# Kernel optimization log

Hardware: AMD Instinct MI355X
Metric: run time of the kernel (lower is better)

The kernel has to match this reference:

```python
import jax, jax.numpy as jnp
import numpy as np

B, T, E = 64, 64, 512
D_MODEL = 2 * E          # 1024, mamba d_model (concat of spatial+temporal)
D_INNER = 2 * D_MODEL    # 2048
D_STATE = 16
DT_RANK = D_MODEL // 16  # 64
K_CONV = 4


def setup_inputs() -> dict:
    key = jax.random.key(0)
    ks = jax.random.split(key, 12)
    def n(k, shape, scale=0.02):
        return jax.random.normal(k, shape, jnp.float32) * scale
    return {
        "spatial_features": jax.random.normal(ks[0], (B, T, E), jnp.float32),
        "temporal_features": jax.random.normal(ks[1], (B, T, E), jnp.float32),
        "W_in": n(ks[2], (D_MODEL, 2 * D_INNER)),
        "conv_w": n(ks[3], (D_INNER, K_CONV)),
        "conv_b": jnp.zeros((D_INNER,), jnp.float32),
        "W_x": n(ks[4], (D_INNER, DT_RANK + 2 * D_STATE)),
        "W_dt": n(ks[5], (DT_RANK, D_INNER)),
        "b_dt": jnp.zeros((D_INNER,), jnp.float32),
        "A_log": n(ks[6], (D_INNER, D_STATE)),   # A = -exp(A_log) ~ -1
        "D_skip": jnp.ones((D_INNER,), jnp.float32),
        "W_out": n(ks[7], (D_INNER, D_MODEL)),
        "W1": n(ks[8], (D_MODEL, 512)),
        "b1": jnp.zeros((512,), jnp.float32),
        "W2": n(ks[9], (512, 256)),
        "b2": jnp.zeros((256,), jnp.float32),
        "W3": n(ks[10], (256, 6)),
        "b3": jnp.zeros((6,), jnp.float32),
    }


def _mamba(x, W_in, conv_w, conv_b, W_x, W_dt, b_dt, A_log, D_skip, W_out):
    # x: (B, T, d_model) -> (B, T, d_model). Standard Mamba selective-scan block.
    Bsz = x.shape[0]
    xz = jnp.einsum('btd,de->bte', x, W_in)            # (B,T,2*d_inner)
    xi, z = jnp.split(xz, 2, axis=-1)
    # causal depthwise conv1d over T
    xt = jnp.pad(jnp.swapaxes(xi, 1, 2), ((0, 0), (0, 0), (K_CONV - 1, 0)))
    conv = jax.lax.conv_general_dilated(
        xt, conv_w[:, None, :], (1,), 'VALID', feature_group_count=D_INNER)
    xc = jax.nn.silu(jnp.swapaxes(conv, 1, 2) + conv_b)  # (B,T,d_inner)
    proj = jnp.einsum('btd,de->bte', xc, W_x)            # (B,T,dt_rank+2n)
    dt_raw, Bs, Cs = jnp.split(proj, [DT_RANK, DT_RANK + D_STATE], axis=-1)
    dt = jax.nn.softplus(jnp.einsum('btr,rd->btd', dt_raw, W_dt) + b_dt)
    A = -jnp.exp(A_log)                                  # (d_inner, n)

    def step(h, inputs):
        dt_t, B_t, C_t, x_t = inputs                     # (B,d),(B,n),(B,n),(B,d)
        dA = jnp.exp(dt_t[..., None] * A)                # (B,d,n)
        h = dA * h + (dt_t * x_t)[..., None] * B_t[:, None, :]
        y = jnp.einsum('bdn,bn->bd', h, C_t)
        return h, y

    xs = (jnp.swapaxes(dt, 0, 1), jnp.swapaxes(Bs, 0, 1),
          jnp.swapaxes(Cs, 0, 1), jnp.swapaxes(xc, 0, 1))
    h0 = jnp.zeros((Bsz, D_INNER, D_STATE), xc.dtype)
    _, ys = jax.lax.scan(step, h0, xs)
    y = jnp.swapaxes(ys, 0, 1) + xc * D_skip
    y = y * jax.nn.silu(z)
    return jnp.einsum('btd,de->bte', y, W_out)


def reference(spatial_features, temporal_features, W_in, conv_w, conv_b, W_x,
              W_dt, b_dt, A_log, D_skip, W_out, W1, b1, W2, b2, W3, b3):
    # concat -> final Mamba -> per-frame MLP head (vectorized over B,T)
    x = jnp.concatenate([spatial_features, temporal_features], axis=-1)  # (B,T,2E)
    f = _mamba(x, W_in, conv_w, conv_b, W_x, W_dt, b_dt, A_log, D_skip, W_out)
    h1 = jax.nn.relu(f @ W1 + b1)
    h2 = jax.nn.relu(h1 @ W2 + b2)
    return h2 @ W3 + b3  # (B,T,6)
```

## Files before the change

kernel.cpp:

```cpp
#include <hip/hip_runtime.h>
#include <hip/hip_bf16.h>
#include <math.h>

#define B_   64
#define T_   64
#define E_   512
#define DM   1024
#define DI   2048
#define DS   16
#define DTR  64
#define M_   4096

typedef __hip_bfloat16 bf16;
typedef __attribute__((ext_vector_type(8))) short bf16x8;
typedef __attribute__((ext_vector_type(4))) float f32x4;

template<int ACT, int OUTBF, int SPLITK, int BM, int BN, int ATOMIC = 0>
__global__ __launch_bounds__(256) void gemm_mfma(
    const bf16* __restrict__ A, int lda,
    const bf16* __restrict__ Bt, int ldb,
    void* __restrict__ Cv, int ldc,
    const float* __restrict__ bias,
    int Ndim, int Kdim)
{
    __shared__ __align__(16) bf16 As[BM * 32];
    __shared__ __align__(16) bf16 Bs[BN * 32];
    const int tid  = threadIdx.x;
    const int wave = tid >> 6;
    const int lane = tid & 63;
    const int bm = blockIdx.y * BM;
    const int bn = blockIdx.x * BN;
    const int lrow = lane >> 2;
    const int lkc  = (lane & 3) * 8;
    constexpr int RPW = (BM + BN) / 4;
    constexpr int NI  = RPW / 16;
    constexpr int WMT = BM / 32;
    constexpr int WNT = BN / 32;
    const int wm = (wave >> 1) * (BM / 2);
    const int wn = (wave & 1) * (BN / 2);
    const int fm = lane & 15;
    const int fq = lane >> 4;

    int kstart = 0, kend = Kdim;
    if (SPLITK > 1) {
        int chunk = Kdim / SPLITK;
        kstart = blockIdx.z * chunk;
        kend = kstart + chunk;
    }

    f32x4 acc[WMT][WNT];
    #pragma unroll
    for (int i = 0; i < WMT; ++i)
        #pragma unroll
        for (int j = 0; j < WNT; ++j)
            acc[i][j] = (f32x4){0.f, 0.f, 0.f, 0.f};

    for (int k0 = kstart; k0 < kend; k0 += 32) {
        #pragma unroll
        for (int i = 0; i < NI; ++i) {
            int rowbase = wave * RPW + i * 16;
            int row = rowbase + lrow;
            if (rowbase < BM) {
                const bf16* ga = A + (size_t)(bm + row) * lda + k0 + lkc;
                __builtin_amdgcn_global_load_lds(
                    (const __attribute__((address_space(1))) void*)ga,
                    (__attribute__((address_space(3))) void*)&As[rowbase * 32],
                    16, 0, 0);
            } else {
                int brow = bn + row - BM;
                if (brow >= Ndim) brow = Ndim - 1;
                const bf16* gb = Bt + (size_t)brow * ldb + k0 + lkc;
                __builtin_amdgcn_global_load_lds(
                    (const __attribute__((address_space(1))) void*)gb,
                    (__attribute__((address_space(3))) void*)&Bs[(rowbase - BM) * 32],
                    16, 0, 0);
            }
        }
        __syncthreads();
        bf16x8 a[WMT], b[WNT];
        #pragma unroll
        for (int i = 0; i < WMT; ++i)
            a[i] = *(const bf16x8*)&As[(wm + i * 16 + fm) * 32 + fq * 8];
        #pragma unroll
        for (int j = 0; j < WNT; ++j)
            b[j] = *(const bf16x8*)&Bs[(wn + j * 16 + fm) * 32 + fq * 8];
        #pragma unroll
        for (int i = 0; i < WMT; ++i)
            #pragma unroll
            for (int j = 0; j < WNT; ++j)
                acc[i][j] = __builtin_amdgcn_mfma_f32_16x16x32_bf16(
                    a[i], b[j], acc[i][j], 0, 0, 0);
        __syncthreads();
    }

    size_t zoff = (SPLITK > 1 && !ATOMIC) ? (size_t)blockIdx.z * M_ * ldc : 0;
    #pragma unroll
    for (int i = 0; i < WMT; ++i) {
        int rowb = bm + wm + i * 16 + fq * 4;
        #pragma unroll
        for (int j = 0; j < WNT; ++j) {
            int col = bn + wn + j * 16 + fm;
            if (col < Ndim) {
                float bv = bias ? bias[col] : 0.f;
                #pragma unroll
                for (int r = 0; r < 4; ++r) {
                    float v = acc[i][j][r] + bv;
                    if (ACT == 1) v = fmaxf(v, 0.f);
                    if (ACT == 2) v = (v > 20.f) ? v : __logf(1.f + __expf(v));
                    size_t off = (size_t)(rowb + r) * ldc + col;
                    if (ATOMIC)          atomicAdd(&((float*)Cv)[off], v);
                    else if (SPLITK > 1) ((float*)Cv)[zoff + off] = v;
                    else if (OUTBF)      ((bf16*)Cv)[off] = __float2bfloat16(v);
                    else                 ((float*)Cv)[off] = v;
                }
            }
        }
    }
}

__global__ __launch_bounds__(256) void gemm_g1_conv(
    const bf16* __restrict__ A,
    const bf16* __restrict__ Bt,
    bf16* __restrict__ xcb,
    bf16* __restrict__ zb,
    const float* __restrict__ conv_w,
    const float* __restrict__ conv_b,
    const bf16* __restrict__ W1T,
    const bf16* __restrict__ Wob,
    bf16* __restrict__ WcT)
{
    constexpr int XS = 136;
    __shared__ __align__(16) bf16 smem[128 * XS];
    const int tid  = threadIdx.x;
    const int wave = tid >> 6;
    const int lane = tid & 63;
    const int lrow = lane >> 2;
    const int lkc  = (lane & 3) * 8;
    const int wm = (wave >> 1) * 64;
    const int fm = lane & 15;
    const int fq = lane >> 4;

    if (blockIdx.x >= 32) {
        const int fbm = (blockIdx.x - 32) * 128;
        const int fbn = blockIdx.y * 64;
        const int fwn = (wave & 1) * 32;
        f32x4 facc[4][2];
        #pragma unroll
        for (int i = 0; i < 4; ++i)
            #pragma unroll
            for (int j = 0; j < 2; ++j)
                facc[i][j] = (f32x4){0.f, 0.f, 0.f, 0.f};

        for (int k0 = 0; k0 < 1024; k0 += 32) {
            #pragma unroll
            for (int i = 0; i < 3; ++i) {
                int rowbase = wave * 48 + i * 16;
                int row = rowbase + lrow;
                if (rowbase < 128) {
                    const bf16* ga = W1T + (size_t)(fbm + row) * 1024 + k0 + lkc;
                    __builtin_amdgcn_global_load_lds(
                        (const __attribute__((address_space(1))) void*)ga,
                        (__attribute__((address_space(3))) void*)&smem[rowbase * 32],
                        16, 0, 0);
                } else {
                    const bf16* gb = Wob + (size_t)(fbn + row - 128) * 1024 + k0 + lkc;
                    __builtin_amdgcn_global_load_lds(
                        (const __attribute__((address_space(1))) void*)gb,
                        (__attribute__((address_space(3))) void*)&smem[4096 + (rowbase - 128) * 32],
                        16, 0, 0);
                }
            }
            __syncthreads();
            bf16x8 a[4], b[2];
            #pragma unroll
            for (int i = 0; i < 4; ++i)
                a[i] = *(const bf16x8*)&smem[(wm + i * 16 + fm) * 32 + fq * 8];
            #pragma unroll
            for (int j = 0; j < 2; ++j)
                b[j] = *(const bf16x8*)&smem[4096 + (fwn + j * 16 + fm) * 32 + fq * 8];
            #pragma unroll
            for (int i = 0; i < 4; ++i)
                #pragma unroll
                for (int j = 0; j < 2; ++j)
                    facc[i][j] = __builtin_amdgcn_mfma_f32_16x16x32_bf16(
                        a[i], b[j], facc[i][j], 0, 0, 0);
            __syncthreads();
        }
        #pragma unroll
        for (int i = 0; i < 4; ++i) {
            int rowb = fbm + wm + i * 16 + fq * 4;
            #pragma unroll
            for (int j = 0; j < 2; ++j) {
                int col = fbn + fwn + j * 16 + fm;
                #pragma unroll
                for (int r = 0; r < 4; ++r)
                    WcT[(size_t)(rowb + r) * 2048 + col] =
                        __float2bfloat16(facc[i][j][r]);
            }
        }
        return;
    }

    const int bm = blockIdx.y * 128;
    const int bn = blockIdx.x * 128;
    const int wn = (wave & 1) * 64;

    f32x4 acc[4][4];
    #pragma unroll
    for (int i = 0; i < 4; ++i)
        #pragma unroll
        for (int j = 0; j < 4; ++j)
            acc[i][j] = (f32x4){0.f, 0.f, 0.f, 0.f};

    for (int k0 = 0; k0 < 1024; k0 += 32) {
        #pragma unroll
        for (int i = 0; i < 4; ++i) {
            int rowbase = wave * 64 + i * 16;
            int row = rowbase + lrow;
            if (rowbase < 128) {
                const bf16* ga = A + (size_t)(bm + row) * 1024 + k0 + lkc;
                __builtin_amdgcn_global_load_lds(
                    (const __attribute__((address_space(1))) void*)ga,
                    (__attribute__((address_space(3))) void*)&smem[rowbase * 32],
                    16, 0, 0);
            } else {
                const bf16* gb = Bt + (size_t)(bn + row - 128) * 1024 + k0 + lkc;
                __builtin_amdgcn_global_load_lds(
                    (const __attribute__((address_space(1))) void*)gb,
                    (__attribute__((address_space(3))) void*)&smem[4096 + (rowbase - 128) * 32],
                    16, 0, 0);
            }
        }
        __syncthreads();
        bf16x8 a[4], b[4];
        #pragma unroll
        for (int i = 0; i < 4; ++i)
            a[i] = *(const bf16x8*)&smem[(wm + i * 16 + fm) * 32 + fq * 8];
        #pragma unroll
        for (int j = 0; j < 4; ++j)
            b[j] = *(const bf16x8*)&smem[4096 + (wn + j * 16 + fm) * 32 + fq * 8];
        #pragma unroll
        for (int i = 0; i < 4; ++i)
            #pragma unroll
            for (int j = 0; j < 4; ++j)
                acc[i][j] = __builtin_amdgcn_mfma_f32_16x16x32_bf16(
                    a[i], b[j], acc[i][j], 0, 0, 0);
        __syncthreads();
    }

    if (bn < 2048) {
        #pragma unroll
        for (int i = 0; i < 4; ++i) {
            int rowb = wm + i * 16 + fq * 4;
            #pragma unroll
            for (int j = 0; j < 4; ++j) {
                int col = wn + j * 16 + fm;
                #pragma unroll
                for (int r = 0; r < 4; ++r)
                    smem[(rowb + r) * XS + col] = __float2bfloat16(acc[i][j][r]);
            }
        }
        __syncthreads();
        {
            int col = tid & 127;
            int seq = tid >> 7;
            int gcol = bn + col;
            float4 cw = *(const float4*)&conv_w[gcol * 4];
            float cb = conv_b[gcol];
            float w0 = 0.f, w1 = 0.f, w2 = 0.f;
            int base = seq * 64;
            for (int t = 0; t < 64; ++t) {
                int idx = (base + t) * XS + col;
                float cur = __bfloat162float(smem[idx]);
                float cacc = cb;
                cacc = fmaf(w0, cw.x, cacc); cacc = fmaf(w1, cw.y, cacc);
                cacc = fmaf(w2, cw.z, cacc); cacc = fmaf(cur, cw.w, cacc);
                smem[idx] = __float2bfloat16(__fdividef(cacc, 1.f + __expf(-cacc)));
                w0 = w1; w1 = w2; w2 = cur;
            }
        }
        __syncthreads();
        #pragma unroll
        for (int it = 0; it < 8; ++it) {
            int g = it * 256 + tid;
            int row = g >> 4;
            int cg = (g & 15) * 8;
            bf16x8 v = *(const bf16x8*)&smem[row * XS + cg];
            *(bf16x8*)&xcb[(size_t)(bm + row) * 2048 + bn + cg] = v;
        }
    } else {
        #pragma unroll
        for (int i = 0; i < 4; ++i) {
            int rowb = bm + wm + i * 16 + fq * 4;
            #pragma unroll
            for (int j = 0; j < 4; ++j) {
                int col = bn - 2048 + wn + j * 16 + fm;
                #pragma unroll
                for (int r = 0; r < 4; ++r)
                    zb[(size_t)(rowb + r) * 2048 + col] =
                        __float2bfloat16(acc[i][j][r]);
            }
        }
    }
}

__global__ __launch_bounds__(256) void gemm_g3(
    const float* __restrict__ proj,
    const bf16* __restrict__ WdT,
    bf16* __restrict__ dtb,
    const float* __restrict__ b_dt)
{
    __shared__ __align__(16) bf16 As[128 * 32];
    __shared__ __align__(16) bf16 Bs[64 * 32];
    const int tid  = threadIdx.x;
    const int wave = tid >> 6;
    const int lane = tid & 63;
    const int bm = blockIdx.y * 128;
    const int bn = blockIdx.x * 64;
    const int lrow = lane >> 2;
    const int lkc  = (lane & 3) * 8;
    const int wm = (wave >> 1) * 64;
    const int wn = (wave & 1) * 32;
    const int fm = lane & 15;
    const int fq = lane >> 4;
    const int arow = tid >> 1;
    const int akh  = (tid & 1) * 16;

    f32x4 acc[4][2];
    #pragma unroll
    for (int i = 0; i < 4; ++i)
        #pragma unroll
        for (int j = 0; j < 2; ++j)
            acc[i][j] = (f32x4){0.f, 0.f, 0.f, 0.f};

    #pragma unroll
    for (int k0 = 0; k0 < 64; k0 += 32) {
        {
            const bf16* gb = WdT + (size_t)(bn + wave * 16 + lrow) * 64 + k0 + lkc;
            __builtin_amdgcn_global_load_lds(
                (const __attribute__((address_space(1))) void*)gb,
                (__attribute__((address_space(3))) void*)&Bs[wave * 16 * 32],
                16, 0, 0);
        }
        {
            const float* ga = proj + (size_t)(bm + arow) * 96 + k0 + akh;
            float4 v0 = *(const float4*)(ga + 0);
            float4 v1 = *(const float4*)(ga + 4);
            float4 v2 = *(const float4*)(ga + 8);
            float4 v3 = *(const float4*)(ga + 12);
            bf16 o[16] = {
                __float2bfloat16(v0.x), __float2bfloat16(v0.y),
                __float2bfloat16(v0.z), __float2bfloat16(v0.w),
                __float2bfloat16(v1.x), __float2bfloat16(v1.y),
                __float2bfloat16(v1.z), __float2bfloat16(v1.w),
                __float2bfloat16(v2.x), __float2bfloat16(v2.y),
                __float2bfloat16(v2.z), __float2bfloat16(v2.w),
                __float2bfloat16(v3.x), __float2bfloat16(v3.y),
                __float2bfloat16(v3.z), __float2bfloat16(v3.w)};
            *(bf16x8*)&As[arow * 32 + akh]     = *(const bf16x8*)&o[0];
            *(bf16x8*)&As[arow * 32 + akh + 8] = *(const bf16x8*)&o[8];
        }
        __syncthreads();
        bf16x8 a[4], b[2];
        #pragma unroll
        for (int i = 0; i < 4; ++i)
            a[i] = *(const bf16x8*)&As[(wm + i * 16 + fm) * 32 + fq * 8];
        #pragma unroll
        for (int j = 0; j < 2; ++j)
            b[j] = *(const bf16x8*)&Bs[(wn + j * 16 + fm) * 32 + fq * 8];
        #pragma unroll
        for (int i = 0; i < 4; ++i)
            #pragma unroll
            for (int j = 0; j < 2; ++j)
                acc[i][j] = __builtin_amdgcn_mfma_f32_16x16x32_bf16(
                    a[i], b[j], acc[i][j], 0, 0, 0);
        __syncthreads();
    }

    #pragma unroll
    for (int i = 0; i < 4; ++i) {
        int rowb = bm + wm + i * 16 + fq * 4;
        #pragma unroll
        for (int j = 0; j < 2; ++j) {
            int col = bn + wn + j * 16 + fm;
            float bv = b_dt[col];
            #pragma unroll
            for (int r = 0; r < 4; ++r) {
                float v = acc[i][j][r] + bv;
                v = (v > 20.f) ? v : __logf(1.f + __expf(v));
                dtb[(size_t)(rowb + r) * 2048 + col] = __float2bfloat16(v);
            }
        }
    }
}

template<int P, int RELU, int NCOL>
__global__ __launch_bounds__(256) void redp_kernel(
    const float* __restrict__ parts, int stride,
    const float* __restrict__ bias, bf16* __restrict__ out)
{
    int i4 = blockIdx.x * 256 + threadIdx.x;
    int i = i4 * 4;
    float4 s = *(const float4*)(parts + i);
    #pragma unroll
    for (int p = 1; p < P; ++p) {
        float4 v = *(const float4*)(parts + (size_t)p * stride + i);
        s.x += v.x; s.y += v.y; s.z += v.z; s.w += v.w;
    }
    if (NCOL > 0) {
        int c = i & (NCOL - 1);
        s.x += bias[c]; s.y += bias[c + 1]; s.z += bias[c + 2]; s.w += bias[c + 3];
    }
    if (RELU) {
        s.x = fmaxf(s.x, 0.f); s.y = fmaxf(s.y, 0.f);
        s.z = fmaxf(s.z, 0.f); s.w = fmaxf(s.w, 0.f);
    }
    bf16 o[4] = {__float2bfloat16(s.x), __float2bfloat16(s.y),
                 __float2bfloat16(s.z), __float2bfloat16(s.w)};
    *(short4*)&out[i] = *(short4*)o;
}

__global__ __launch_bounds__(256) void prep_kernel(
    const float* __restrict__ sp, const float* __restrict__ tp,
    bf16* __restrict__ xb, float* __restrict__ proj,
    const float* __restrict__ W_in,  bf16* __restrict__ WinT,
    const float* __restrict__ W_out, bf16* __restrict__ Wob,
    const float* __restrict__ W_x,   bf16* __restrict__ WxT,
    const float* __restrict__ W_dt,  bf16* __restrict__ WdT,
    const float* __restrict__ W1,    bf16* __restrict__ W1T,
    const float* __restrict__ W2,    bf16* __restrict__ W2T)
{
    __shared__ float tile[32][33];
    const int b = blockIdx.x;
    const int tid = threadIdx.x;
    if (b < 4096) {
        int idx = b * 256 + tid;
        int row = idx >> 8;
        int c4 = (idx & 255) * 4;
        const float* src = (c4 < 512) ? (sp + (size_t)row * 512 + c4)
                                      : (tp + (size_t)row * 512 + (c4 - 512));
        float4 v = *(const float4*)src;
        bf16* dst = xb + (size_t)row * 1024 + c4;
        dst[0] = __float2bfloat16(v.x); dst[1] = __float2bfloat16(v.y);
        dst[2] = __float2bfloat16(v.z); dst[3] = __float2bfloat16(v.w);
        if (idx < 98304)
            *(float4*)(proj + (size_t)idx * 4) = make_float4(0.f, 0.f, 0.f, 0.f);
        return;
    }
    if (b < 6144) {
        int idx = (b - 4096) * 1024 + tid * 4;
        float4 v = *(const float4*)(W_out + idx);
        bf16 o[4] = {__float2bfloat16(v.x), __float2bfloat16(v.y),
                     __float2bfloat16(v.z), __float2bfloat16(v.w)};
        *(short4*)&Wob[idx] = *(short4*)o;
        return;
    }
    const float* W; bf16* Wt; int K, N, tb;
    if      (b < 6336) { W = W_x;  Wt = WxT;  K = 2048; N = 96;   tb = b - 6144; }
    else if (b < 6464) { W = W_dt; Wt = WdT;  K = 64;   N = 2048; tb = b - 6336; }
    else if (b < 6976) { W = W1;   Wt = W1T;  K = 1024; N = 512;  tb = b - 6464; }
    else if (b < 7104) { W = W2;   Wt = W2T;  K = 512;  N = 256;  tb = b - 6976; }
    else               { W = W_in; Wt = WinT; K = 1024; N = 4096; tb = b - 7104; }
    int nb = N / 32;
    int bn = (tb % nb) * 32, bk = (tb / nb) * 32;
    int tx = tid & 31, ty = tid >> 5;
    #pragma unroll
    for (int i = 0; i < 32; i += 8)
        tile[ty + i][tx] = W[(size_t)(bk + ty + i) * N + bn + tx];
    __syncthreads();
    #pragma unroll
    for (int i = 0; i < 32; i += 8)
        Wt[(size_t)(bn + ty + i) * K + bk + tx] = __float2bfloat16(tile[tx][ty + i]);
}

__global__ __launch_bounds__(256) void scan_kernel(
    const float* __restrict__ proj,
    const bf16*  __restrict__ dtb,
    bf16* __restrict__ xcy,
    const bf16*  __restrict__ zb,
    const float* __restrict__ A_log,
    const float* __restrict__ D_skip)
{
    __shared__ float BC[64][32];
    const int tid = threadIdx.x;
    const int b = blockIdx.y;
    for (int i = tid; i < 64 * 32; i += 256) {
        int t = i >> 5, c = i & 31;
        BC[t][c] = proj[(size_t)(b * 64 + t) * 96 + 64 + c];
    }
    __syncthreads();

    const int d = blockIdx.x * 256 + tid;
    float av[16];
    const float4* alp = (const float4*)(A_log + d * 16);
    *(float4*)&av[0]  = alp[0];
    *(float4*)&av[4]  = alp[1];
    *(float4*)&av[8]  = alp[2];
    *(float4*)&av[12] = alp[3];
    float A[16];
    #pragma unroll
    for (int n = 0; n < 16; ++n) A[n] = -__expf(av[n]);
    const float Dv = D_skip[d];
    float h[16];
    #pragma unroll
    for (int n = 0; n < 16; ++n) h[n] = 0.f;

    #pragma unroll 2
    for (int t = 0; t < T_; ++t) {
        int row = b * T_ + t;
        size_t off = (size_t)row * DI + d;
        float xv = __bfloat162float(xcy[off]);
        float dt = __bfloat162float(dtb[off]);
        float dtx = dt * xv;
        float y = 0.f;
        #pragma unroll
        for (int n = 0; n < 16; ++n) {
            float dA = __expf(dt * A[n]);
            h[n] = fmaf(dA, h[n], dtx * BC[t][n]);
            y = fmaf(h[n], BC[t][16 + n], y);
        }
        float sk = fmaf(xv, Dv, y);
        float z = __bfloat162float(zb[off]);
        float g = __fdividef(z, 1.f + __expf(-z));
        xcy[off] = __float2bfloat16(sk * g);
    }
}

template<int P>
__global__ __launch_bounds__(256) void head_kernel(
    const float* __restrict__ p6, int stride,
    const float* __restrict__ b2,
    const float* __restrict__ W3, const float* __restrict__ b3,
    float* __restrict__ out)
{
    int row = blockIdx.x * 4 + (threadIdx.x >> 6);
    int lane = threadIdx.x & 63;
    float acc[6] = {0.f, 0.f, 0.f, 0.f, 0.f, 0.f};
    #pragma unroll
    for (int kk = 0; kk < 4; ++kk) {
        int c = lane + kk * 64;
        size_t off = (size_t)row * 256 + c;
        float s = p6[off];
        #pragma unroll
        for (int p = 1; p < P; ++p) s += p6[(size_t)p * stride + off];
        s = fmaxf(s + b2[c], 0.f);
        #pragma unroll
        for (int n = 0; n < 6; ++n) acc[n] = fmaf(s, W3[c * 6 + n], acc[n]);
    }
    #pragma unroll
    for (int n = 0; n < 6; ++n) {
        float v = acc[n];
        #pragma unroll
        for (int off = 32; off > 0; off >>= 1) v += __shfl_down(v, off);
        if (lane == 0) out[(size_t)row * 6 + n] = v + b3[n];
    }
}

extern "C" void kernel_launch(void* const* d_in, const int* in_sizes, int n_in,
                              void* d_out, int out_size, void* d_ws, size_t ws_size,
                              hipStream_t stream)
{
    const float* spatial  = (const float*)d_in[0];
    const float* temporal = (const float*)d_in[1];
    const float* W_in     = (const float*)d_in[2];
    const float* conv_w   = (const float*)d_in[3];
    const float* conv_b   = (const float*)d_in[4];
    const float* W_x      = (const float*)d_in[5];
    const float* W_dt     = (const float*)d_in[6];
    const float* b_dt     = (const float*)d_in[7];
    const float* A_log    = (const float*)d_in[8];
    const float* D_skip   = (const float*)d_in[9];
    const float* W_out    = (const float*)d_in[10];
    const float* W1       = (const float*)d_in[11];
    const float* b1       = (const float*)d_in[12];
    const float* W2       = (const float*)d_in[13];
    const float* b2       = (const float*)d_in[14];
    const float* W3       = (const float*)d_in[15];
    const float* b3       = (const float*)d_in[16];
    float* out = (float*)d_out;

    char* w = (char*)d_ws;
    bf16*  xcb  = (bf16*)(w);
    bf16*  zb   = (bf16*)(w + 16777216);
    bf16*  dtb  = (bf16*)(w + 33554432);
    float* p5   = (float*)(w + 33554432);
    float* p6   = (float*)(w + 33554432);
    bf16*  xb   = (bf16*)(w + 67108864);
    bf16*  WinT = (bf16*)(w + 75497472);
    bf16*  WcT  = (bf16*)(w + 83886080);
    bf16*  W1T  = (bf16*)(w + 88080384);
    bf16*  W2T  = (bf16*)(w + 89128960);
    bf16*  WxT  = (bf16*)(w + 89391104);
    bf16*  WdT  = (bf16*)(w + 89784320);
    float* proj = (float*)(w + 90046464);
    bf16*  h1   = (bf16*)(w + 91619328);
    bf16*  Wob  = (bf16*)(w + 95813632);

    dim3 blk(256);

    prep_kernel<<<dim3(11200), blk, 0, stream>>>(
        spatial, temporal, xb, proj, W_in, WinT, W_out, Wob,
        W_x, WxT, W_dt, WdT, W1, W1T, W2, W2T);

    gemm_g1_conv<<<dim3(36, 32), blk, 0, stream>>>(
        xb, WinT, xcb, zb, conv_w, conv_b, W1T, Wob, WcT);

    gemm_mfma<0, 0, 8, 128, 128, 1><<<dim3(1, 32, 8), blk, 0, stream>>>(
        xcb, 2048, WxT, 2048, proj, 96, nullptr, 96, 2048);

    gemm_g3<<<dim3(32, 32), blk, 0, stream>>>(proj, WdT, dtb, b_dt);

    scan_kernel<<<dim3(8, 64), blk, 0, stream>>>(
        proj, dtb, xcb, zb, A_log, D_skip);

    gemm_mfma<0, 0, 2, 128, 128><<<dim3(4, 32, 2), blk, 0, stream>>>(
        xcb, 2048, WcT, 2048, p5, 512, nullptr, 512, 2048);

    redp_kernel<2, 1, 512><<<dim3(2048), blk, 0, stream>>>(
        p5, 2097152, b1, h1);

    gemm_mfma<0, 0, 4, 128, 128><<<dim3(2, 32, 4), blk, 0, stream>>>(
        h1, 512, W2T, 512, p6, 256, nullptr, 256, 512);

    head_kernel<4><<<dim3(1024), blk, 0, stream>>>(
        p6, 1048576, b2, W3, b3, out);
}
```

Before: 299.0 us.

## Fuse dt projection into scan kernel and split-K reduce into W2 GEMM

```diff
diff --git a/kernel.cpp b/kernel.cpp
--- a/kernel.cpp
+++ b/kernel.cpp
@@ -15,12 +15,11 @@
 typedef __attribute__((ext_vector_type(8))) short bf16x8;
 typedef __attribute__((ext_vector_type(4))) float f32x4;
 
-template<int ACT, int OUTBF, int SPLITK, int BM, int BN, int ATOMIC = 0>
+template<int SPLITK, int BM, int BN, int ATOMIC = 0>
 __global__ __launch_bounds__(256) void gemm_mfma(
     const bf16* __restrict__ A, int lda,
     const bf16* __restrict__ Bt, int ldb,
-    void* __restrict__ Cv, int ldc,
-    const float* __restrict__ bias,
+    float* __restrict__ Cv, int ldc,
     int Ndim, int Kdim)
 {
     __shared__ __align__(16) bf16 As[BM * 32];
@@ -101,17 +100,12 @@
         for (int j = 0; j < WNT; ++j) {
             int col = bn + wn + j * 16 + fm;
             if (col < Ndim) {
-                float bv = bias ? bias[col] : 0.f;
                 #pragma unroll
                 for (int r = 0; r < 4; ++r) {
-                    float v = acc[i][j][r] + bv;
-                    if (ACT == 1) v = fmaxf(v, 0.f);
-                    if (ACT == 2) v = (v > 20.f) ? v : __logf(1.f + __expf(v));
+                    float v = acc[i][j][r];
                     size_t off = (size_t)(rowb + r) * ldc + col;
-                    if (ATOMIC)          atomicAdd(&((float*)Cv)[off], v);
-                    else if (SPLITK > 1) ((float*)Cv)[zoff + off] = v;
-                    else if (OUTBF)      ((bf16*)Cv)[off] = __float2bfloat16(v);
-                    else                 ((float*)Cv)[off] = v;
+                    if (ATOMIC) atomicAdd(&Cv[off], v);
+                    else        Cv[zoff + off] = v;
                 }
             }
         }
@@ -304,120 +298,222 @@
     }
 }
 
-__global__ __launch_bounds__(256) void gemm_g3(
+__global__ __launch_bounds__(256) void scan_g3_kernel(
     const float* __restrict__ proj,
-    const bf16* __restrict__ WdT,
-    bf16* __restrict__ dtb,
-    const float* __restrict__ b_dt)
+    const bf16*  __restrict__ WdT,
+    const float* __restrict__ b_dt,
+    bf16* __restrict__ xcy,
+    const bf16*  __restrict__ zb,
+    const float* __restrict__ A_log,
+    const float* __restrict__ D_skip)
+{
+    __shared__ float BC[64][32];
+    __shared__ __align__(16) bf16 Adt[64 * 64];
+    __shared__ __align__(16) bf16 Bdt[256 * 64];
+    const int tid  = threadIdx.x;
+    const int wave = tid >> 6;
+    const int lane = tid & 63;
+    const int b  = blockIdx.y;
+    const int dg = blockIdx.x;
+    const int fm = lane & 15;
+    const int fq = lane >> 4;
+
+    for (int i = tid; i < 64 * 32; i += 256) {
+        int t = i >> 5, c = i & 31;
+        BC[t][c] = proj[(size_t)(b * 64 + t) * 96 + 64 + c];
+    }
+    {
+        int arow = tid >> 2;
+        int ak = (tid & 3) * 16;
+        const float* ga = proj + (size_t)(b * 64 + arow) * 96 + ak;
+        float4 v0 = *(const float4*)(ga + 0);
+        float4 v1 = *(const float4*)(ga + 4);
+        float4 v2 = *(const float4*)(ga + 8);
+        float4 v3 = *(const float4*)(ga + 12);
+        bf16 o[16] = {
+            __float2bfloat16(v0.x), __float2bfloat16(v0.y),
+            __float2bfloat16(v0.z), __float2bfloat16(v0.w),
+            __float2bfloat16(v1.x), __float2bfloat16(v1.y),
+            __float2bfloat16(v1.z), __float2bfloat16(v1.w),
+            __float2bfloat16(v2.x), __float2bfloat16(v2.y),
+            __float2bfloat16(v2.z), __float2bfloat16(v2.w),
+            __float2bfloat16(v3.x), __float2bfloat16(v3.y),
+            __float2bfloat16(v3.z), __float2bfloat16(v3.w)};
+        *(bf16x8*)&Adt[arow * 64 + ak]     = *(const bf16x8*)&o[0];
+        *(bf16x8*)&Adt[arow * 64 + ak + 8] = *(const bf16x8*)&o[8];
+    }
+    #pragma unroll
+    for (int i = 0; i < 8; ++i) {
+        int rowbase = wave * 64 + i * 8;
+        const bf16* gb = WdT + (size_t)(dg * 256 + rowbase + (lane >> 3)) * 64
+                             + (lane & 7) * 8;
+        __builtin_amdgcn_global_load_lds(
+            (const __attribute__((address_space(1))) void*)gb,
+            (__attribute__((address_space(3))) void*)&Bdt[rowbase * 64],
+            16, 0, 0);
+    }
+    __syncthreads();
+
+    f32x4 acc[4][4];
+    #pragma unroll
+    for (int i = 0; i < 4; ++i)
+        #pragma unroll
+        for (int j = 0; j < 4; ++j)
+            acc[i][j] = (f32x4){0.f, 0.f, 0.f, 0.f};
+    #pragma unroll
+    for (int k0 = 0; k0 < 64; k0 += 32) {
+        bf16x8 a[4], bfr[4];
+        #pragma unroll
+        for (int i = 0; i < 4; ++i)
+            a[i] = *(const bf16x8*)&Adt[(i * 16 + fm) * 64 + k0 + fq * 8];
+        #pragma unroll
+        for (int j = 0; j < 4; ++j)
+            bfr[j] = *(const bf16x8*)&Bdt[(wave * 64 + j * 16 + fm) * 64 + k0 + fq * 8];
+        #pragma unroll
+        for (int i = 0; i < 4; ++i)
+            #pragma unroll
+            for (int j = 0; j < 4; ++j)
+                acc[i][j] = __builtin_amdgcn_mfma_f32_16x16x32_bf16(
+                    a[i], bfr[j], acc[i][j], 0, 0, 0);
+    }
+    __syncthreads();
+    bf16* dt_s = Bdt;
+    #pragma unroll
+    for (int j = 0; j < 4; ++j) {
+        int dloc = wave * 64 + j * 16 + fm;
+        float bv = b_dt[dg * 256 + dloc];
+        #pragma unroll
+        for (int i = 0; i < 4; ++i) {
+            #pragma unroll
+            for (int r = 0; r < 4; ++r) {
+                int t = i * 16 + fq * 4 + r;
+                float v = acc[i][j][r] + bv;
+                v = (v > 20.f) ? v : __logf(1.f + __expf(v));
+                dt_s[t * 256 + dloc] = __float2bfloat16(v);
+            }
+        }
+    }
+    __syncthreads();
+
+    const int d = dg * 256 + tid;
+    float av[16];
+    const float4* alp = (const float4*)(A_log + d * 16);
+    *(float4*)&av[0]  = alp[0];
+    *(float4*)&av[4]  = alp[1];
+    *(float4*)&av[8]  = alp[2];
+    *(float4*)&av[12] = alp[3];
+    float A[16];
+    #pragma unroll
+    for (int n = 0; n < 16; ++n) A[n] = -__expf(av[n]);
+    const float Dv = D_skip[d];
+    float h[16];
+    #pragma unroll
+    for (int n = 0; n < 16; ++n) h[n] = 0.f;
+
+    #pragma unroll 2
+    for (int t = 0; t < T_; ++t) {
+        int row = b * T_ + t;
+        size_t off = (size_t)row * DI + d;
+        float xv = __bfloat162float(xcy[off]);
+        float dt = __bfloat162float(dt_s[t * 256 + tid]);
+        float dtx = dt * xv;
+        float y = 0.f;
+        #pragma unroll
+        for (int n = 0; n < 16; ++n) {
+            float dA = __expf(dt * A[n]);
+            h[n] = fmaf(dA, h[n], dtx * BC[t][n]);
+            y = fmaf(h[n], BC[t][16 + n], y);
+        }
+        float sk = fmaf(xv, Dv, y);
+        float z = __bfloat162float(zb[off]);
+        float g = __fdividef(z, 1.f + __expf(-z));
+        xcy[off] = __float2bfloat16(sk * g);
+    }
+}
+
+__global__ __launch_bounds__(256) void gemm_g6(
+    const float* __restrict__ p5,
+    const bf16* __restrict__ W2T,
+    float* __restrict__ p6,
+    const float* __restrict__ b1)
 {
     __shared__ __align__(16) bf16 As[128 * 32];
-    __shared__ __align__(16) bf16 Bs[64 * 32];
+    __shared__ __align__(16) bf16 Bs[128 * 32];
     const int tid  = threadIdx.x;
     const int wave = tid >> 6;
     const int lane = tid & 63;
     const int bm = blockIdx.y * 128;
-    const int bn = blockIdx.x * 64;
+    const int bn = blockIdx.x * 128;
     const int lrow = lane >> 2;
     const int lkc  = (lane & 3) * 8;
     const int wm = (wave >> 1) * 64;
-    const int wn = (wave & 1) * 32;
+    const int wn = (wave & 1) * 64;
     const int fm = lane & 15;
     const int fq = lane >> 4;
-    const int arow = tid >> 1;
-    const int akh  = (tid & 1) * 16;
-
-    f32x4 acc[4][2];
+    const int kstart = blockIdx.z * 128;
+
+    f32x4 acc[4][4];
     #pragma unroll
     for (int i = 0; i < 4; ++i)
         #pragma unroll
-        for (int j = 0; j < 2; ++j)
+        for (int j = 0; j < 4; ++j)
             acc[i][j] = (f32x4){0.f, 0.f, 0.f, 0.f};
 
-    #pragma unroll
-    for (int k0 = 0; k0 < 64; k0 += 32) {
-        {
-            const bf16* gb = WdT + (size_t)(bn + wave * 16 + lrow) * 64 + k0 + lkc;
+    for (int k0 = kstart; k0 < kstart + 128; k0 += 32) {
+        #pragma unroll
+        for (int i = 0; i < 2; ++i) {
+            int rowbase = wave * 32 + i * 16;
+            const bf16* gb = W2T + (size_t)(bn + rowbase + lrow) * 512 + k0 + lkc;
             __builtin_amdgcn_global_load_lds(
                 (const __attribute__((address_space(1))) void*)gb,
-                (__attribute__((address_space(3))) void*)&Bs[wave * 16 * 32],
+                (__attribute__((address_space(3))) void*)&Bs[rowbase * 32],
                 16, 0, 0);
         }
-        {
-            const float* ga = proj + (size_t)(bm + arow) * 96 + k0 + akh;
-            float4 v0 = *(const float4*)(ga + 0);
-            float4 v1 = *(const float4*)(ga + 4);
-            float4 v2 = *(const float4*)(ga + 8);
-            float4 v3 = *(const float4*)(ga + 12);
-            bf16 o[16] = {
-                __float2bfloat16(v0.x), __float2bfloat16(v0.y),
-                __float2bfloat16(v0.z), __float2bfloat16(v0.w),
-                __float2bfloat16(v1.x), __float2bfloat16(v1.y),
-                __float2bfloat16(v1.z), __float2bfloat16(v1.w),
-                __float2bfloat16(v2.x), __float2bfloat16(v2.y),
-                __float2bfloat16(v2.z), __float2bfloat16(v2.w),
-                __float2bfloat16(v3.x), __float2bfloat16(v3.y),
-                __float2bfloat16(v3.z), __float2bfloat16(v3.w)};
-            *(bf16x8*)&As[arow * 32 + akh]     = *(const bf16x8*)&o[0];
-            *(bf16x8*)&As[arow * 32 + akh + 8] = *(const bf16x8*)&o[8];
-        }
-        __syncthreads();
-        bf16x8 a[4], b[2];
+        #pragma unroll
+        for (int p = 0; p < 4; ++p) {
+            int idx = p * 256 + tid;
+            int arow = idx >> 3;
+            int ak4 = (idx & 7) * 4;
+            const float* ga = p5 + (size_t)(bm + arow) * 512 + k0 + ak4;
+            float4 u = *(const float4*)ga;
+            float4 v = *(const float4*)(ga + 2097152);
+            float4 bb = *(const float4*)(b1 + k0 + ak4);
+            bf16 o[4] = {
+                __float2bfloat16(fmaxf(u.x + v.x + bb.x, 0.f)),
+                __float2bfloat16(fmaxf(u.y + v.y + bb.y, 0.f)),
+                __float2bfloat16(fmaxf(u.z + v.z + bb.z, 0.f)),
+                __float2bfloat16(fmaxf(u.w + v.w + bb.w, 0.f))};
+            *(short4*)&As[arow * 32 + ak4] = *(const short4*)o;
+        }
+        __syncthreads();
+        bf16x8 a[4], b[4];
         #pragma unroll
         for (int i = 0; i < 4; ++i)
             a[i] = *(const bf16x8*)&As[(wm + i * 16 + fm) * 32 + fq * 8];
         #pragma unroll
-        for (int j = 0; j < 2; ++j)
+        for (int j = 0; j < 4; ++j)
             b[j] = *(const bf16x8*)&Bs[(wn + j * 16 + fm) * 32 + fq * 8];
         #pragma unroll
         for (int i = 0; i < 4; ++i)
             #pragma unroll
-            for (int j = 0; j < 2; ++j)
+            for (int j = 0; j < 4; ++j)
                 acc[i][j] = __builtin_amdgcn_mfma_f32_16x16x32_bf16(
                     a[i], b[j], acc[i][j], 0, 0, 0);
         __syncthreads();
     }
 
+    size_t zoff = (size_t)blockIdx.z * M_ * 256;
     #pragma unroll
     for (int i = 0; i < 4; ++i) {
         int rowb = bm + wm + i * 16 + fq * 4;
         #pragma unroll
-        for (int j = 0; j < 2; ++j) {
+        for (int j = 0; j < 4; ++j) {
             int col = bn + wn + j * 16 + fm;
-            float bv = b_dt[col];
-            #pragma unroll
-            for (int r = 0; r < 4; ++r) {
-                float v = acc[i][j][r] + bv;
-                v = (v > 20.f) ? v : __logf(1.f + __expf(v));
-                dtb[(size_t)(rowb + r) * 2048 + col] = __float2bfloat16(v);
-            }
-        }
-    }
-}
-
-template<int P, int RELU, int NCOL>
-__global__ __launch_bounds__(256) void redp_kernel(
-    const float* __restrict__ parts, int stride,
-    const float* __restrict__ bias, bf16* __restrict__ out)
-{
-    int i4 = blockIdx.x * 256 + threadIdx.x;
-    int i = i4 * 4;
-    float4 s = *(const float4*)(parts + i);
-    #pragma unroll
-    for (int p = 1; p < P; ++p) {
-        float4 v = *(const float4*)(parts + (size_t)p * stride + i);
-        s.x += v.x; s.y += v.y; s.z += v.z; s.w += v.w;
-    }
-    if (NCOL > 0) {
-        int c = i & (NCOL - 1);
-        s.x += bias[c]; s.y += bias[c + 1]; s.z += bias[c + 2]; s.w += bias[c + 3];
-    }
-    if (RELU) {
-        s.x = fmaxf(s.x, 0.f); s.y = fmaxf(s.y, 0.f);
-        s.z = fmaxf(s.z, 0.f); s.w = fmaxf(s.w, 0.f);
-    }
-    bf16 o[4] = {__float2bfloat16(s.x), __float2bfloat16(s.y),
-                 __float2bfloat16(s.z), __float2bfloat16(s.w)};
-    *(short4*)&out[i] = *(short4*)o;
+            #pragma unroll
+            for (int r = 0; r < 4; ++r)
+                p6[zoff + (size_t)(rowb + r) * 256 + col] = acc[i][j][r];
+        }
+    }
 }
 
 __global__ __launch_bounds__(256) void prep_kernel(
@@ -473,59 +569,6 @@
         Wt[(size_t)(bn + ty + i) * K + bk + tx] = __float2bfloat16(tile[tx][ty + i]);
 }
 
-__global__ __launch_bounds__(256) void scan_kernel(
-    const float* __restrict__ proj,
-    const bf16*  __restrict__ dtb,
-    bf16* __restrict__ xcy,
-    const bf16*  __restrict__ zb,
-    const float* __restrict__ A_log,
-    const float* __restrict__ D_skip)
-{
-    __shared__ float BC[64][32];
-    const int tid = threadIdx.x;
-    const int b = blockIdx.y;
-    for (int i = tid; i < 64 * 32; i += 256) {
-        int t = i >> 5, c = i & 31;
-        BC[t][c] = proj[(size_t)(b * 64 + t) * 96 + 64 + c];
-    }
-    __syncthreads();
-
-    const int d = blockIdx.x * 256 + tid;
-    float av[16];
-    const float4* alp = (const float4*)(A_log + d * 16);
-    *(float4*)&av[0]  = alp[0];
-    *(float4*)&av[4]  = alp[1];
-    *(float4*)&av[8]  = alp[2];
-    *(float4*)&av[12] = alp[3];
-    float A[16];
-    #pragma unroll
-    for (int n = 0; n < 16; ++n) A[n] = -__expf(av[n]);
-    const float Dv = D_skip[d];
-    float h[16];
-    #pragma unroll
-    for (int n = 0; n < 16; ++n) h[n] = 0.f;
-
-    #pragma unroll 2
-    for (int t = 0; t < T_; ++t) {
-        int row = b * T_ + t;
-        size_t off = (size_t)row * DI + d;
-        float xv = __bfloat162float(xcy[off]);
-        float dt = __bfloat162float(dtb[off]);
-        float dtx = dt * xv;
-        float y = 0.f;
-        #pragma unroll
-        for (int n = 0; n < 16; ++n) {
-            float dA = __expf(dt * A[n]);
-            h[n] = fmaf(dA, h[n], dtx * BC[t][n]);
-            y = fmaf(h[n], BC[t][16 + n], y);
-        }
-        float sk = fmaf(xv, Dv, y);
-        float z = __bfloat162float(zb[off]);
-        float g = __fdividef(z, 1.f + __expf(-z));
-        xcy[off] = __float2bfloat16(sk * g);
-    }
-}
-
 template<int P>
 __global__ __launch_bounds__(256) void head_kernel(
     const float* __restrict__ p6, int stride,
@@ -582,19 +625,17 @@
     char* w = (char*)d_ws;
     bf16*  xcb  = (bf16*)(w);
     bf16*  zb   = (bf16*)(w + 16777216);
-    bf16*  dtb  = (bf16*)(w + 33554432);
     float* p5   = (float*)(w + 33554432);
-    float* p6   = (float*)(w + 33554432);
+    float* p6   = (float*)(w + 50331648);
     bf16*  xb   = (bf16*)(w + 67108864);
     bf16*  WinT = (bf16*)(w + 75497472);
     bf16*  WcT  = (bf16*)(w + 83886080);
-    bf16*  W1T  = (bf16*)(w + 88080384);
-    bf16*  W2T  = (bf16*)(w + 89128960);
-    bf16*  WxT  = (bf16*)(w + 89391104);
-    bf16*  WdT  = (bf16*)(w + 89784320);
-    float* proj = (float*)(w + 90046464);
-    bf16*  h1   = (bf16*)(w + 91619328);
-    bf16*  Wob  = (bf16*)(w + 95813632);
+    bf16*  W1T  = (bf16*)(w + 85983232);
+    bf16*  W2T  = (bf16*)(w + 87031808);
+    bf16*  WxT  = (bf16*)(w + 87293952);
+    bf16*  WdT  = (bf16*)(w + 87687168);
+    float* proj = (float*)(w + 87949312);
+    bf16*  Wob  = (bf16*)(w + 89522176);
 
     dim3 blk(256);
 
@@ -605,22 +646,16 @@
     gemm_g1_conv<<<dim3(36, 32), blk, 0, stream>>>(
         xb, WinT, xcb, zb, conv_w, conv_b, W1T, Wob, WcT);
 
-    gemm_mfma<0, 0, 8, 128, 128, 1><<<dim3(1, 32, 8), blk, 0, stream>>>(
-        xcb, 2048, WxT, 2048, proj, 96, nullptr, 96, 2048);
-
-    gemm_g3<<<dim3(32, 32), blk, 0, stream>>>(proj, WdT, dtb, b_dt);
-
-    scan_kernel<<<dim3(8, 64), blk, 0, stream>>>(
-        proj, dtb, xcb, zb, A_log, D_skip);
-
-    gemm_mfma<0, 0, 2, 128, 128><<<dim3(4, 32, 2), blk, 0, stream>>>(
-        xcb, 2048, WcT, 2048, p5, 512, nullptr, 512, 2048);
-
-    redp_kernel<2, 1, 512><<<dim3(2048), blk, 0, stream>>>(
-        p5, 2097152, b1, h1);
-
-    gemm_mfma<0, 0, 4, 128, 128><<<dim3(2, 32, 4), blk, 0, stream>>>(
-        h1, 512, W2T, 512, p6, 256, nullptr, 256, 512);
+    gemm_mfma<8, 128, 128, 1><<<dim3(1, 32, 8), blk, 0, stream>>>(
+        xcb, 2048, WxT, 2048, proj, 96, 96, 2048);
+
+    scan_g3_kernel<<<dim3(8, 64), blk, 0, stream>>>(
+        proj, WdT, b_dt, xcb, zb, A_log, D_skip);
+
+    gemm_mfma<2, 128, 128><<<dim3(4, 32, 2), blk, 0, stream>>>(
+        xcb, 2048, WcT, 2048, p5, 512, 512, 2048);
+
+    gemm_g6<<<dim3(2, 32, 4), blk, 0, stream>>>(p5, W2T, p6, b1);
 
     head_kernel<4><<<dim3(1024), blk, 0, stream>>>(
         p6, 1048576, b2, W3, b3, out);
```

Measured after the change: 277.7 us. -7.1%, faster.
